# Performance work log

Measured on AMD Instinct MI355X. Metric: run time of the kernel, lower is better.

## Reference

```python
import jax, jax.numpy as jnp
import numpy as np

EPS = 1e-6
ALPHA = 0.2  # LeakyReLU negative slope


def layer_norm(x, g, b):
    mu = jnp.mean(x, axis=-1, keepdims=True)
    var = jnp.mean(jnp.square(x - mu), axis=-1, keepdims=True)
    return (x - mu) * jax.lax.rsqrt(var + EPS) * g + b


def graph_attention(x, bias, W, a_src, a_dst):
    # x: [B,N,D], bias: [B,N,N], W: [D, H*Dh], a_src/a_dst: [H, Dh]
    B, N, D = x.shape
    H, Dh = a_src.shape
    h = jnp.einsum('bnd,dhk->bhnk', x, W.reshape(D, H, Dh))  # [B,H,N,Dh]
    s = jnp.einsum('bhnk,hk->bhn', h, a_src)                 # source term
    t = jnp.einsum('bhnk,hk->bhn', h, a_dst)                 # target term
    e = jax.nn.leaky_relu(s[:, :, :, None] + t[:, :, None, :], ALPHA)
    e = e + bias[:, None, :, :]                              # graph mask/bias
    attn = jax.nn.softmax(e, axis=-1)                        # [B,H,N,N]
    out = jnp.einsum('bhij,bhjk->bhik', attn, h)             # [B,H,N,Dh]
    return out.transpose(0, 2, 1, 3).reshape(B, N, H * Dh)


def setup_inputs() -> dict:
    key = jax.random.key(0)
    ks = jax.random.split(key, 8)
    B, N, D, H = 2, 2048, 512, 8
    Dh = D // H
    sc = 1.0 / np.sqrt(D)
    return {
        'x': jax.random.normal(ks[0], (B, N, D), jnp.float32),
        'bias': jax.random.normal(ks[1], (B, N, N), jnp.float32),
        'W1': jax.random.normal(ks[2], (D, D), jnp.float32) * sc,
        'a_src1': jax.random.normal(ks[3], (H, Dh), jnp.float32) * sc,
        'a_dst1': jax.random.normal(ks[4], (H, Dh), jnp.float32) * sc,
        'g1': jnp.ones((D,), jnp.float32),
        'b1': jnp.zeros((D,), jnp.float32),
        'W2': jax.random.normal(ks[5], (D, D), jnp.float32) * sc,
        'a_src2': jax.random.normal(ks[6], (1, D), jnp.float32) * sc,
        'a_dst2': jax.random.normal(ks[7], (1, D), jnp.float32) * sc,
        'g2': jnp.ones((D,), jnp.float32),
        'b2': jnp.zeros((D,), jnp.float32),
    }


def reference(x, bias, W1, a_src1, a_dst1, g1, b1, W2, a_src2, a_dst2, g2, b2):
    # dropout is identity in eval mode
    attn_in = layer_norm(x, g1, b1)
    attn = graph_attention(attn_in, bias, W1, a_src1, a_dst1) + x
    attn_in2 = layer_norm(attn, g2, b2)
    out = graph_attention(attn_in2, bias, W2, a_src2, a_dst2) + attn
    return out
```

## Files before the change

### kernel.cpp

```cpp
#include <hip/hip_runtime.h>
#include <math.h>

#define NB 2
#define NN 2048
#define DD 512

typedef __attribute__((ext_vector_type(8))) short short8;
typedef __attribute__((ext_vector_type(4))) float f32x4;

__device__ __forceinline__ unsigned short f2bf(float x) {
  union { float f; unsigned u; } a;
  a.f = x;
  unsigned r = a.u + 0x7FFF + ((a.u >> 16) & 1);
  return (unsigned short)(r >> 16);
}
__device__ __forceinline__ float bf2f(unsigned short u) {
  union { unsigned u; float f; } a;
  a.u = ((unsigned)u) << 16;
  return a.f;
}
__device__ __forceinline__ unsigned cvtpk(float lo, float hi) {
  unsigned r;
  asm("v_cvt_pk_bf16_f32 %0, %1, %2" : "=v"(r) : "v"(lo), "v"(hi));
  return r;
}

__device__ __forceinline__ float waveReduceSum(float v) {
#pragma unroll
  for (int o = 32; o; o >>= 1) v += __shfl_down(v, o, 64);
  return v;
}
__device__ __forceinline__ float blockReduceSum(float v, float* red4) {
  int tid = threadIdx.x;
  __syncthreads();
  v = waveReduceSum(v);
  if ((tid & 63) == 0) red4[tid >> 6] = v;
  __syncthreads();
  return red4[0] + red4[1] + red4[2] + red4[3];
}

__global__ __launch_bounds__(256) void ln_kernel(const float* __restrict__ x,
                                                 const float* __restrict__ g,
                                                 const float* __restrict__ bb,
                                                 unsigned short* __restrict__ y) {
  int row = blockIdx.x;
  int t = threadIdx.x;
  const float* xr = x + (size_t)row * DD;
  __shared__ float red4[4];
  float2 v = *(const float2*)&xr[2 * t];
  float s = blockReduceSum(v.x + v.y, red4);
  float mu = s * (1.0f / 512.0f);
  float d0 = v.x - mu, d1 = v.y - mu;
  float ss = blockReduceSum(d0 * d0 + d1 * d1, red4);
  float rstd = rsqrtf(ss * (1.0f / 512.0f) + 1e-6f);
  float2 gg = *(const float2*)&g[2 * t];
  float2 bv = *(const float2*)&bb[2 * t];
  ushort2 o;
  o.x = f2bf(d0 * rstd * gg.x + bv.x);
  o.y = f2bf(d1 * rstd * gg.y + bv.y);
  *(ushort2*)&y[(size_t)row * DD + 2 * t] = o;
}

__global__ __launch_bounds__(256) void wt2_kernel(const float* __restrict__ W1,
                                                  const float* __restrict__ W2,
                                                  unsigned short* __restrict__ WT1,
                                                  unsigned short* __restrict__ WT2) {
  const float* W = blockIdx.z ? W2 : W1;
  unsigned short* WT = blockIdx.z ? WT2 : WT1;
  __shared__ float tile[64][65];
  int kt = blockIdx.x * 64, ct = blockIdx.y * 64;
  int t = threadIdx.x;
#pragma unroll
  for (int u = 0; u < 16; u++) {
    int lin = t + u * 256;
    int kl = lin >> 6, cl = lin & 63;
    tile[kl][cl] = W[(size_t)(kt + kl) * DD + ct + cl];
  }
  __syncthreads();
#pragma unroll
  for (int u = 0; u < 16; u++) {
    int lin = t + u * 256;
    int cl = lin >> 6, kl = lin & 63;
    WT[(size_t)(ct + cl) * DD + kt + kl] = f2bf(tile[kl][cl]);
  }
}

__global__ __launch_bounds__(256) void v2_kernel(
    const float* __restrict__ W1, const float* __restrict__ as1,
    const float* __restrict__ ad1, float* __restrict__ vs1, float* __restrict__ vd1,
    const float* __restrict__ W2, const float* __restrict__ as2,
    const float* __restrict__ ad2, float* __restrict__ vs2, float* __restrict__ vd2) {
  int slot = blockIdx.y;
  const float *W, *as, *ad;
  float *vs, *vd;
  int Dh, hoff;
  if (slot < 8) {
    W = W1; as = as1 + slot * 64; ad = ad1 + slot * 64;
    vs = vs1 + (size_t)slot * DD; vd = vd1 + (size_t)slot * DD;
    Dh = 64; hoff = slot * 64;
  } else {
    W = W2; as = as2; ad = ad2; vs = vs2; vd = vd2;
    Dh = 512; hoff = 0;
  }
  int t = threadIdx.x;
  int dl = t >> 2, kq = t & 3;
  int d = blockIdx.x * 64 + dl;
  int kn = Dh >> 2;
  const float* wr = W + (size_t)d * DD + hoff + kq * kn;
  const float* asp = as + kq * kn;
  const float* adp = ad + kq * kn;
  float s = 0.f, dd2 = 0.f;
  for (int k = 0; k < kn; k++) {
    float wv = wr[k];
    s += wv * asp[k];
    dd2 += wv * adp[k];
  }
  s += __shfl_xor(s, 1);
  s += __shfl_xor(s, 2);
  dd2 += __shfl_xor(dd2, 1);
  dd2 += __shfl_xor(dd2, 2);
  if (kq == 0) {
    vs[d] = s;
    vd[d] = dd2;
  }
}

__global__ __launch_bounds__(256) void biasH_kernel(const float* __restrict__ bias,
                                                    unsigned short* __restrict__ biasH) {
  int row = blockIdx.x;
  int t = threadIdx.x;
  const float* br = bias + (size_t)row * NN;
  float4 a = *(const float4*)&br[t * 4];
  float4 c = *(const float4*)&br[t * 4 + 1024];
  uint2 d0, d1;
  d0.x = cvtpk(a.x, a.y);
  d0.y = cvtpk(a.z, a.w);
  d1.x = cvtpk(c.x, c.y);
  d1.y = cvtpk(c.z, c.w);
  *(uint2*)&biasH[(size_t)row * NN + t * 4] = d0;
  *(uint2*)&biasH[(size_t)row * NN + t * 4 + 1024] = d1;
}

__global__ __launch_bounds__(256) void gemm_kernel(const unsigned short* __restrict__ A,
                                                   const unsigned short* __restrict__ BT,
                                                   unsigned short* __restrict__ hbT) {
  __shared__ float accL[4][16][65];
  int t = threadIdx.x, w = t >> 6, l = t & 63;
  int li = l & 15, lg = l >> 4;
  int R0 = blockIdx.x * 16;
  int c0 = blockIdx.y * 64;
  const unsigned short* ar = A + (size_t)(R0 + li) * DD + w * 128 + lg * 8;
  const unsigned short* br = BT + (size_t)(c0 + li) * DD + w * 128 + lg * 8;
  f32x4 acc[4] = {};
#pragma unroll
  for (int k0 = 0; k0 < 128; k0 += 32) {
    short8 af = *(const short8*)(ar + k0);
#pragma unroll
    for (int f = 0; f < 4; f++) {
      short8 bf = *(const short8*)(br + (size_t)f * 16 * DD + k0);
      acc[f] = __builtin_amdgcn_mfma_f32_16x16x32_bf16(af, bf, acc[f], 0, 0, 0);
    }
  }
#pragma unroll
  for (int f = 0; f < 4; f++)
#pragma unroll
    for (int r = 0; r < 4; r++) accL[w][lg * 4 + r][f * 16 + li] = acc[f][r];
  __syncthreads();
  int b = R0 >> 11, jT = (R0 & (NN - 1)) >> 4;
#pragma unroll
  for (int u = 0; u < 2; u++) {
    int idx = t + u * 256;
    int f = idx >> 7;
    int rem = idx & 127;
    int cl = rem >> 3, jlp = rem & 7;
    int cc = f * 16 + cl;
    float v0 = accL[0][2 * jlp][cc] + accL[1][2 * jlp][cc] + accL[2][2 * jlp][cc] +
               accL[3][2 * jlp][cc];
    float v1 = accL[0][2 * jlp + 1][cc] + accL[1][2 * jlp + 1][cc] +
               accL[2][2 * jlp + 1][cc] + accL[3][2 * jlp + 1][cc];
    size_t off = (((size_t)(b * (DD / 64) + blockIdx.y) * (NN / 16)) + jT) * 1024 +
                 f * 256 + cl * 16 + jlp * 2;
    *(unsigned*)(hbT + off) = cvtpk(v0, v1);
  }
}

__global__ __launch_bounds__(256) void st_kernel(const unsigned short* __restrict__ lnB,
                                                 const float* __restrict__ vs,
                                                 const float* __restrict__ vd,
                                                 float* __restrict__ sOut,
                                                 float* __restrict__ tOut, int HN) {
  int t = threadIdx.x, w = t >> 6, l = t & 63;
  int row = blockIdx.x * 4 + w;
  int b = row >> 11, n = row & (NN - 1);
  const unsigned short* lr = lnB + (size_t)row * DD + l * 8;
  union { short8 v; unsigned short u[8]; } xv;
  xv.v = *(const short8*)lr;
  float xf[8];
#pragma unroll
  for (int k = 0; k < 8; k++) xf[k] = bf2f(xv.u[k]);
  for (int h = 0; h < HN; h++) {
    const float* vsr = vs + (size_t)h * DD + l * 8;
    const float* vdr = vd + (size_t)h * DD + l * 8;
    float4 a0 = *(const float4*)vsr, a1 = *(const float4*)(vsr + 4);
    float4 c0 = *(const float4*)vdr, c1 = *(const float4*)(vdr + 4);
    float ps = xf[0] * a0.x + xf[1] * a0.y + xf[2] * a0.z + xf[3] * a0.w +
               xf[4] * a1.x + xf[5] * a1.y + xf[6] * a1.z + xf[7] * a1.w;
    float pd = xf[0] * c0.x + xf[1] * c0.y + xf[2] * c0.z + xf[3] * c0.w +
               xf[4] * c1.x + xf[5] * c1.y + xf[6] * c1.z + xf[7] * c1.w;
#pragma unroll
    for (int o = 32; o; o >>= 1) {
      ps += __shfl_xor(ps, o);
      pd += __shfl_xor(pd, o);
    }
    if (l == 0) {
      sOut[((size_t)b * HN + h) * NN + n] = ps;
      tOut[((size_t)b * HN + h) * NN + n] = pd;
    }
  }
}

template <int HN, int CCH>
__global__ __launch_bounds__(256) void pv_kernel(
    const unsigned short* __restrict__ hbT, const unsigned short* __restrict__ biasH,
    const float* __restrict__ sArr, const float* __restrict__ tArr,
    const float* __restrict__ res, float* __restrict__ out) {
  constexpr int DH = DD / HN;
  __shared__ unsigned short Pl[4][512];
  __shared__ float accL[4][16][33];
  __shared__ float sLa[4][16];
  int t = threadIdx.x, w = t >> 6, l = t & 63;
  int li = l & 15, lg = l >> 4;
  int i0 = blockIdx.x * 16;
  int ck = blockIdx.y, bh = blockIdx.z;
  int h = bh % HN, b = bh / HN;
  int c0 = h * DH + ck * (CCH * 64);
  size_t bhN = (size_t)bh * NN;
  const float* trow = tArr + bhN;

  int rs = l >> 3;
  int js = (l & 7) * 4;
  int wq = (((l & 7) >> 1) ^ (rs & 3)) * 8 + (l & 1) * 4;
  float sv[2];
  sv[0] = sArr[bhN + i0 + rs];
  sv[1] = sArr[bhN + i0 + 8 + rs];
  const unsigned short* bb0 = biasH + ((size_t)b * NN + i0 + rs) * NN;
  const unsigned short* bb1 = bb0 + (size_t)8 * NN;

  const unsigned short* vbase =
      hbT + ((size_t)(b * (DD / 64) + (c0 >> 6)) * (NN / 16)) * 1024 +
      (lg >> 1) * 1024 + li * 16 + (lg & 1) * 8;
  int ra0 = li * 32 + ((lg ^ (li & 3)) * 8);

  union { short8 v; unsigned short q[8]; } ones;
#pragma unroll
  for (int k = 0; k < 8; k++) ones.q[k] = 0x3F80;

  const int jbeg = w * (NN / 4), jend = jbeg + NN / 4;
  f32x4 acc[CCH][4] = {};
  f32x4 accS = {0.f, 0.f, 0.f, 0.f};

  float4 ptv = *(const float4*)&trow[jbeg + js];
  uint2 pq0 = *(const uint2*)&bb0[jbeg + js];
  uint2 pq1 = *(const uint2*)&bb1[jbeg + js];
  short8 nv[CCH][4];
#pragma unroll
  for (int cc = 0; cc < CCH; cc++) {
    const unsigned short* vp = vbase + (size_t)cc * ((NN / 16) * 1024) + (size_t)jbeg * 64;
#pragma unroll
    for (int f = 0; f < 4; f++) nv[cc][f] = *(const short8*)(vp + f * 256);
  }

  for (int jt = jbeg; jt < jend; jt += 32) {
    float4 tv = ptv;
    uint2 bq0 = pq0, bq1 = pq1;
    short8 v[CCH][4];
#pragma unroll
    for (int cc = 0; cc < CCH; cc++)
#pragma unroll
      for (int f = 0; f < 4; f++) v[cc][f] = nv[cc][f];
    if (jt + 32 < jend) {
      int jb = jt + 32 + js;
      ptv = *(const float4*)&trow[jb];
      pq0 = *(const uint2*)&bb0[jb];
      pq1 = *(const uint2*)&bb1[jb];
#pragma unroll
      for (int cc = 0; cc < CCH; cc++) {
        const unsigned short* vp =
            vbase + (size_t)cc * ((NN / 16) * 1024) + (size_t)(jt + 32) * 64;
#pragma unroll
        for (int f = 0; f < 4; f++) nv[cc][f] = *(const short8*)(vp + f * 256);
      }
    }
#pragma unroll
    for (int u = 0; u < 2; u++) {
      union { uint2 v; unsigned short q[4]; } bu;
      bu.v = u ? bq1 : bq0;
      int row = u * 8 + rs;
      float e0 = sv[u] + tv.x;
      float e1 = sv[u] + tv.y;
      float e2 = sv[u] + tv.z;
      float e3 = sv[u] + tv.w;
      e0 = fmaxf(e0, 0.2f * e0) + bf2f(bu.q[0]);
      e1 = fmaxf(e1, 0.2f * e1) + bf2f(bu.q[1]);
      e2 = fmaxf(e2, 0.2f * e2) + bf2f(bu.q[2]);
      e3 = fmaxf(e3, 0.2f * e3) + bf2f(bu.q[3]);
      uint2 d;
      d.x = cvtpk(__expf(e0), __expf(e1));
      d.y = cvtpk(__expf(e2), __expf(e3));
      *(uint2*)&Pl[w][row * 32 + wq] = d;
    }
    short8 a0 = *(const short8*)&Pl[w][ra0];
    __builtin_amdgcn_s_setprio(1);
    accS = __builtin_amdgcn_mfma_f32_16x16x32_bf16(a0, ones.v, accS, 0, 0, 0);
#pragma unroll
    for (int cc = 0; cc < CCH; cc++)
#pragma unroll
      for (int f = 0; f < 4; f++)
        acc[cc][f] = __builtin_amdgcn_mfma_f32_16x16x32_bf16(a0, v[cc][f], acc[cc][f], 0, 0, 0);
    __builtin_amdgcn_s_setprio(0);
  }
  if (li == 0) {
#pragma unroll
    for (int r = 0; r < 4; r++) sLa[w][lg * 4 + r] = accS[r];
  }
#pragma unroll
  for (int g = 0; g < 2 * CCH; g++) {
    int cc = g >> 1, half = g & 1;
#pragma unroll
    for (int f = 0; f < 2; f++)
#pragma unroll
      for (int r = 0; r < 4; r++)
        accL[w][lg * 4 + r][f * 16 + li] = acc[cc][half * 2 + f][r];
    __syncthreads();
    {
      int rr = t >> 4, cp = (t & 15) * 2;
      float S = sLa[0][rr] + sLa[1][rr] + sLa[2][rr] + sLa[3][rr];
      float inv = 1.0f / S;
      float2 O = {0.f, 0.f};
#pragma unroll
      for (int w2 = 0; w2 < 4; w2++) {
        O.x += accL[w2][rr][cp];
        O.y += accL[w2][rr][cp + 1];
      }
      size_t ix = ((size_t)b * NN + i0 + rr) * DD + c0 + cc * 64 + half * 32 + cp;
      float2 rv = *(const float2*)&res[ix];
      float2 ov = {O.x * inv + rv.x, O.y * inv + rv.y};
      *(float2*)&out[ix] = ov;
    }
    __syncthreads();
  }
}

extern "C" void kernel_launch(void* const* d_in, const int* in_sizes, int n_in,
                              void* d_out, int out_size, void* d_ws, size_t ws_size,
                              hipStream_t stream) {
  const float* x = (const float*)d_in[0];
  const float* bias = (const float*)d_in[1];
  const float* W1 = (const float*)d_in[2];
  const float* asrc1 = (const float*)d_in[3];
  const float* adst1 = (const float*)d_in[4];
  const float* g1 = (const float*)d_in[5];
  const float* b1 = (const float*)d_in[6];
  const float* W2 = (const float*)d_in[7];
  const float* asrc2 = (const float*)d_in[8];
  const float* adst2 = (const float*)d_in[9];
  const float* g2 = (const float*)d_in[10];
  const float* b2 = (const float*)d_in[11];
  float* out = (float*)d_out;
  float* ws = (float*)d_ws;

  const size_t RC = (size_t)NB * NN * DD;
  float* attnBuf = ws;
  unsigned short* lnB = (unsigned short*)(ws + RC);
  unsigned short* hbT = (unsigned short*)(ws + RC + RC / 2);
  unsigned short* WT1 = (unsigned short*)(ws + 2 * RC);
  unsigned short* WT2 = WT1 + (size_t)DD * DD;
  float* vs1 = (float*)(WT2 + (size_t)DD * DD);
  float* vd1 = vs1 + 8 * DD;
  float* vs2 = vd1 + 8 * DD;
  float* vd2 = vs2 + DD;
  float* sBuf = vd2 + DD;
  float* tBuf = sBuf + 16 * NN;
  unsigned short* biasH = (unsigned short*)(tBuf + 16 * NN);

  const int rows = NB * NN;

  hipLaunchKernelGGL(wt2_kernel, dim3(8, 8, 2), dim3(256), 0, stream, W1, W2, WT1, WT2);
  hipLaunchKernelGGL(v2_kernel, dim3(8, 9), dim3(256), 0, stream, W1, asrc1, adst1, vs1, vd1,
                     W2, asrc2, adst2, vs2, vd2);
  hipLaunchKernelGGL(biasH_kernel, dim3(rows), dim3(256), 0, stream, bias, biasH);

  hipLaunchKernelGGL(ln_kernel, dim3(rows), dim3(256), 0, stream, x, g1, b1, lnB);
  hipLaunchKernelGGL(gemm_kernel, dim3(256, 8), dim3(256), 0, stream, lnB, WT1, hbT);
  hipLaunchKernelGGL(st_kernel, dim3(rows / 4), dim3(256), 0, stream, lnB, vs1, vd1, sBuf, tBuf, 8);
  hipLaunchKernelGGL((pv_kernel<8, 1>), dim3(128, 1, 16), dim3(256), 0, stream, hbT, biasH,
                     sBuf, tBuf, x, attnBuf);

  hipLaunchKernelGGL(ln_kernel, dim3(rows), dim3(256), 0, stream, attnBuf, g2, b2, lnB);
  hipLaunchKernelGGL(gemm_kernel, dim3(256, 8), dim3(256), 0, stream, lnB, WT2, hbT);
  hipLaunchKernelGGL(st_kernel, dim3(rows / 4), dim3(256), 0, stream, lnB, vs2, vd2, sBuf, tBuf, 1);
  hipLaunchKernelGGL((pv_kernel<1, 2>), dim3(128, 4, 2), dim3(256), 0, stream, hbT, biasH,
                     sBuf, tBuf, attnBuf, out);
}
```

Measured before the change: 167.2 us.

## Double-buffer P tiles and fold log2e into exp inputs in pv kernel

```diff
diff --git a/kernel.cpp b/kernel.cpp
--- a/kernel.cpp
+++ b/kernel.cpp
@@ -4,9 +4,11 @@
 #define NB 2
 #define NN 2048
 #define DD 512
+#define L2E 1.44269504088896340736f
 
 typedef __attribute__((ext_vector_type(8))) short short8;
 typedef __attribute__((ext_vector_type(4))) float f32x4;
+typedef __attribute__((ext_vector_type(2))) float f32x2;
 
 __device__ __forceinline__ unsigned short f2bf(float x) {
   union { float f; unsigned u; } a;
@@ -23,6 +25,19 @@
   unsigned r;
   asm("v_cvt_pk_bf16_f32 %0, %1, %2" : "=v"(r) : "v"(lo), "v"(hi));
   return r;
+}
+__device__ __forceinline__ uint2 exp4pk(float e0, float e1, float e2, float e3) {
+  float p0, p1, p2, p3;
+  uint2 d;
+  asm("v_exp_f32 %2, %6\n\t"
+      "v_exp_f32 %3, %7\n\t"
+      "v_exp_f32 %4, %8\n\t"
+      "v_exp_f32 %5, %9\n\t"
+      "v_cvt_pk_bf16_f32 %0, %2, %3\n\t"
+      "v_cvt_pk_bf16_f32 %1, %4, %5"
+      : "=&v"(d.x), "=&v"(d.y), "=&v"(p0), "=&v"(p1), "=&v"(p2), "=&v"(p3)
+      : "v"(e0), "v"(e1), "v"(e2), "v"(e3));
+  return d;
 }
 
 __device__ __forceinline__ float waveReduceSum(float v) {
@@ -133,10 +148,10 @@
   float4 a = *(const float4*)&br[t * 4];
   float4 c = *(const float4*)&br[t * 4 + 1024];
   uint2 d0, d1;
-  d0.x = cvtpk(a.x, a.y);
-  d0.y = cvtpk(a.z, a.w);
-  d1.x = cvtpk(c.x, c.y);
-  d1.y = cvtpk(c.z, c.w);
+  d0.x = cvtpk(a.x * L2E, a.y * L2E);
+  d0.y = cvtpk(a.z * L2E, a.w * L2E);
+  d1.x = cvtpk(c.x * L2E, c.y * L2E);
+  d1.y = cvtpk(c.z * L2E, c.w * L2E);
   *(uint2*)&biasH[(size_t)row * NN + t * 4] = d0;
   *(uint2*)&biasH[(size_t)row * NN + t * 4 + 1024] = d1;
 }
@@ -213,8 +228,8 @@
       pd += __shfl_xor(pd, o);
     }
     if (l == 0) {
-      sOut[((size_t)b * HN + h) * NN + n] = ps;
-      tOut[((size_t)b * HN + h) * NN + n] = pd;
+      sOut[((size_t)b * HN + h) * NN + n] = ps * L2E;
+      tOut[((size_t)b * HN + h) * NN + n] = pd * L2E;
     }
   }
 }
@@ -225,7 +240,7 @@
     const float* __restrict__ sArr, const float* __restrict__ tArr,
     const float* __restrict__ res, float* __restrict__ out) {
   constexpr int DH = DD / HN;
-  __shared__ unsigned short Pl[4][512];
+  __shared__ unsigned short Pl[4][2][512];
   __shared__ float accL[4][16][33];
   __shared__ float sLa[4][16];
   int t = threadIdx.x, w = t >> 6, l = t & 63;
@@ -259,66 +274,74 @@
   f32x4 acc[CCH][4] = {};
   f32x4 accS = {0.f, 0.f, 0.f, 0.f};
 
-  float4 ptv = *(const float4*)&trow[jbeg + js];
-  uint2 pq0 = *(const uint2*)&bb0[jbeg + js];
-  uint2 pq1 = *(const uint2*)&bb1[jbeg + js];
-  short8 nv[CCH][4];
-#pragma unroll
-  for (int cc = 0; cc < CCH; cc++) {
-    const unsigned short* vp = vbase + (size_t)cc * ((NN / 16) * 1024) + (size_t)jbeg * 64;
-#pragma unroll
-    for (int f = 0; f < 4; f++) nv[cc][f] = *(const short8*)(vp + f * 256);
-  }
-
-  for (int jt = jbeg; jt < jend; jt += 32) {
-    float4 tv = ptv;
-    uint2 bq0 = pq0, bq1 = pq1;
-    short8 v[CCH][4];
-#pragma unroll
-    for (int cc = 0; cc < CCH; cc++)
-#pragma unroll
-      for (int f = 0; f < 4; f++) v[cc][f] = nv[cc][f];
-    if (jt + 32 < jend) {
-      int jb = jt + 32 + js;
-      ptv = *(const float4*)&trow[jb];
-      pq0 = *(const uint2*)&bb0[jb];
-      pq1 = *(const uint2*)&bb1[jb];
-#pragma unroll
-      for (int cc = 0; cc < CCH; cc++) {
-        const unsigned short* vp =
-            vbase + (size_t)cc * ((NN / 16) * 1024) + (size_t)(jt + 32) * 64;
-#pragma unroll
-        for (int f = 0; f < 4; f++) nv[cc][f] = *(const short8*)(vp + f * 256);
-      }
-    }
+  auto loadTB = [&](int j, float4& tv, uint2& q0, uint2& q1) {
+    tv = *(const float4*)&trow[j + js];
+    q0 = *(const uint2*)&bb0[j + js];
+    q1 = *(const uint2*)&bb1[j + js];
+  };
+  auto loadV = [&](int j, short8 (&vv)[CCH][4]) {
+#pragma unroll
+    for (int cc = 0; cc < CCH; cc++) {
+      const unsigned short* vp =
+          vbase + (size_t)cc * ((NN / 16) * 1024) + (size_t)j * 64;
+#pragma unroll
+      for (int f = 0; f < 4; f++) vv[cc][f] = *(const short8*)(vp + f * 256);
+    }
+  };
+  auto computeP = [&](const float4& tv, uint2 q0, uint2 q1, int pb) {
+    f32x2 t01 = {tv.x, tv.y}, t23 = {tv.z, tv.w};
 #pragma unroll
     for (int u = 0; u < 2; u++) {
-      union { uint2 v; unsigned short q[4]; } bu;
-      bu.v = u ? bq1 : bq0;
+      uint2 qu = u ? q1 : q0;
       int row = u * 8 + rs;
-      float e0 = sv[u] + tv.x;
-      float e1 = sv[u] + tv.y;
-      float e2 = sv[u] + tv.z;
-      float e3 = sv[u] + tv.w;
-      e0 = fmaxf(e0, 0.2f * e0) + bf2f(bu.q[0]);
-      e1 = fmaxf(e1, 0.2f * e1) + bf2f(bu.q[1]);
-      e2 = fmaxf(e2, 0.2f * e2) + bf2f(bu.q[2]);
-      e3 = fmaxf(e3, 0.2f * e3) + bf2f(bu.q[3]);
-      uint2 d;
-      d.x = cvtpk(__expf(e0), __expf(e1));
-      d.y = cvtpk(__expf(e2), __expf(e3));
-      *(uint2*)&Pl[w][row * 32 + wq] = d;
-    }
-    short8 a0 = *(const short8*)&Pl[w][ra0];
+      f32x2 s2 = {sv[u], sv[u]};
+      f32x2 e01 = s2 + t01, e23 = s2 + t23;
+      e01 = __builtin_elementwise_max(e01, e01 * 0.2f);
+      e23 = __builtin_elementwise_max(e23, e23 * 0.2f);
+      f32x2 b01 = {__uint_as_float(qu.x << 16), __uint_as_float(qu.x & 0xFFFF0000u)};
+      f32x2 b23 = {__uint_as_float(qu.y << 16), __uint_as_float(qu.y & 0xFFFF0000u)};
+      e01 += b01;
+      e23 += b23;
+      uint2 d = exp4pk(e01.x, e01.y, e23.x, e23.y);
+      *(uint2*)&Pl[w][pb][row * 32 + wq] = d;
+    }
+  };
+  auto domfma = [&](short8 a0, const short8 (&vv)[CCH][4]) {
     __builtin_amdgcn_s_setprio(1);
     accS = __builtin_amdgcn_mfma_f32_16x16x32_bf16(a0, ones.v, accS, 0, 0, 0);
 #pragma unroll
     for (int cc = 0; cc < CCH; cc++)
 #pragma unroll
       for (int f = 0; f < 4; f++)
-        acc[cc][f] = __builtin_amdgcn_mfma_f32_16x16x32_bf16(a0, v[cc][f], acc[cc][f], 0, 0, 0);
+        acc[cc][f] =
+            __builtin_amdgcn_mfma_f32_16x16x32_bf16(a0, vv[cc][f], acc[cc][f], 0, 0, 0);
     __builtin_amdgcn_s_setprio(0);
-  }
+  };
+
+  float4 tvA, tvB;
+  uint2 qA0, qA1, qB0, qB1;
+  short8 vA[CCH][4], vB[CCH][4];
+
+  loadTB(jbeg, tvA, qA0, qA1);
+  computeP(tvA, qA0, qA1, 0);
+  loadTB(jbeg + 32, tvA, qA0, qA1);
+  loadV(jbeg, vA);
+
+  for (int jt = jbeg; jt < jend; jt += 64) {
+    short8 a0 = *(const short8*)&Pl[w][0][ra0];
+    loadV(jt + 32, vB);
+    loadTB(jt + 64, tvB, qB0, qB1);
+    computeP(tvA, qA0, qA1, 1);
+    domfma(a0, vA);
+    short8 a1 = *(const short8*)&Pl[w][1][ra0];
+    if (jt + 64 < jend) {
+      loadV(jt + 64, vA);
+      loadTB(jt + 96, tvA, qA0, qA1);
+      computeP(tvB, qB0, qB1, 0);
+    }
+    domfma(a1, vB);
+  }
+
   if (li == 0) {
 #pragma unroll
     for (int r = 0; r < 4; r++) sLa[w][lg * 4 + r] = accS[r];
```

Result: no change. 165.9 us (-0.8%).
